# Kernel tuning notes

Hardware: AMD Instinct MI355X
Metric: run time of the kernel (lower is better)

## Reference

```python
import jax, jax.numpy as jnp
from jax import lax
import numpy as np

T, B, C, H, L, K = 512, 32, 512, 512, 2, 2  # time, batch, in_feat, hidden, layers, kernel


def setup_inputs() -> dict:
    key = jax.random.key(0)
    k0, k1, k2 = jax.random.split(key, 3)
    x = jax.random.normal(k0, (T, B, C), dtype=jnp.float32)
    # per layer: [n_dir=2, n_gate=4 (z,f,o,i), H, Cin, K] conv weights and [2,4,H] biases
    w0 = jax.random.normal(k1, (2, 4, H, C, K), dtype=jnp.float32) * 0.05
    b0 = jnp.zeros((2, 4, H), dtype=jnp.float32)
    w1 = jax.random.normal(k2, (2, 4, H, 2 * H, K), dtype=jnp.float32) * 0.05
    b1 = jnp.zeros((2, 4, H), dtype=jnp.float32)
    return {"x": x, "w0": w0, "b0": b0, "w1": w1, "b1": b1}


def _conv(x, w, b):
    # x: [B, Cin, T], w: [H, Cin, K]; left-pad K-1 zeros == torch cat([zeros, x]) + VALID conv
    y = lax.conv_general_dilated(x, w, (1,), [(K - 1, 0)],
                                 dimension_numbers=("NCH", "OIH", "NCH"))
    return y + b[None, :, None]


def _qrnn_layer(x, W, b, reverse):
    # x: [B, Cin, T]; W: [4, H, Cin, K]; b: [4, H]
    if reverse:
        x = x[:, :, ::-1]  # note: original code does NOT flip the output back
    z = jnp.tanh(_conv(x, W[0], b[0]))
    f = jax.nn.sigmoid(_conv(x, W[1], b[1]))  # eval-mode zoneout: 1-(1-sigmoid)=sigmoid
    o = jax.nn.sigmoid(_conv(x, W[2], b[2]))
    i = jax.nn.sigmoid(_conv(x, W[3], b[3]))
    iz = i * z
    f_t = jnp.moveaxis(f, 2, 0)   # [T, B, H]
    iz_t = jnp.moveaxis(iz, 2, 0)

    def step(c, fi):
        ft, izt = fi
        c = ft * c + izt  # IFO pooling recurrence
        return c, c

    _, cs = lax.scan(step, jnp.zeros(f_t.shape[1:], f.dtype), (f_t, iz_t))
    c = jnp.moveaxis(cs, 0, 2)  # [B, H, T]
    return o * c


def _forward(x, w0, b0, w1, b1):
    h = jnp.transpose(x, (1, 2, 0))  # [T,B,C] -> [B,C,T]
    h_lasts = []
    for W, bb in ((w0, b0), (w1, b1)):
        d0 = _qrnn_layer(h, W[0], bb[0], False)
        d1 = _qrnn_layer(h, W[1], bb[1], True)
        t_last = h.shape[2] - 2  # lengths.fill_(T-1); t_last = lengths - 1 = T-2 (faithful)
        h_lasts.append(jnp.concatenate([d0[:, :, t_last], d1[:, :, 0]], axis=1))  # [B, 2H]
        h = jnp.concatenate([d0, d1], axis=1)  # [B, 2H, T]
    output = jnp.transpose(h, (2, 0, 1))  # [T, B, 2H]
    h_n = jnp.stack(h_lasts, axis=0)      # [L, B, 2H]
    return output, h_n


def reference(x, w0, b0, w1, b1):
    return _forward(x, w0, b0, w1, b1)
```

## Files before the change

kernel.cpp:

```cpp
#include <hip/hip_runtime.h>
#include <cstddef>
#include <cstdint>

#define Tn 512
#define Bn 32
#define Hn 512
static const size_t PLANE = 8388608;

typedef float f32x4 __attribute__((ext_vector_type(4)));
typedef __bf16 bf16x8 __attribute__((ext_vector_type(8)));
typedef _Float16 h2 __attribute__((ext_vector_type(2)));

__device__ __forceinline__ float sigm(float x) { return 1.0f / (1.0f + __expf(-x)); }
__device__ __forceinline__ float tanh_fast(float x) { return 2.0f / (1.0f + __expf(-2.0f * x)) - 1.0f; }
__device__ __forceinline__ unsigned short f2bf(float f) {
    unsigned int u = __float_as_uint(f);
    u += 0x7FFF + ((u >> 16) & 1);
    return (unsigned short)(u >> 16);
}


__global__ __launch_bounds__(256) void conv_x(const float* __restrict__ x,
                                              unsigned short* __restrict__ xbf) {
    const int i = blockIdx.x * 256 + threadIdx.x;
    const int c8 = i & 63;
    const int tp = (i >> 6) % 514;
    const int b  = (i >> 6) / 514;
    unsigned short v[8];
    if (tp == 0 || tp == 513) {
#pragma unroll
        for (int j = 0; j < 8; ++j) v[j] = 0;
    } else {
        const float* s = x + ((size_t)(tp - 1) * Bn + b) * 512 + c8 * 8;
#pragma unroll
        for (int j = 0; j < 8; ++j) v[j] = f2bf(s[j]);
    }
    unsigned short* d = xbf + ((size_t)b * 514 + tp) * 512 + c8 * 8;
    *(uint4*)d = *(const uint4*)v;
}

__global__ __launch_bounds__(256) void conv_w2(const float* __restrict__ w0,
                                               const float* __restrict__ w1,
                                               unsigned short* __restrict__ w0bf,
                                               unsigned short* __restrict__ w1bf) {
    int i = blockIdx.x * 256 + threadIdx.x;
    const float* src;
    unsigned short* dst;
    int Cin;
    if (i < 4194304) { src = w0; dst = w0bf; Cin = 512; }
    else { i -= 4194304; src = w1; dst = w1bf; Cin = 1024; }
    const int K = 2 * Cin;
    const int dm2 = i / K;
    const int kp = i - dm2 * K;
    const int dir = dm2 >> 11;
    const int mp = dm2 & 2047;
    const int o = mp >> 2;
    const int g = mp & 3;
    const int tap = (kp >= Cin) ? 1 : 0;
    const int c = kp - tap * Cin;
    dst[i] = f2bf(src[((((size_t)dir * 4 + g) * 512 + o) * Cin + c) * 2 + tap]);
}

__global__ __launch_bounds__(256) void zero_h1pad(unsigned short* __restrict__ h1bf) {
    const int i = blockIdx.x * 256 + threadIdx.x;
    const int c = i & 1023;
    const int b = (i >> 10) & 31;
    const int tp = (i >> 15) ? 513 : 0;
    h1bf[((size_t)b * 514 + tp) * 1024 + c] = 0;
}

template <int CIN>
__global__ __launch_bounds__(512, 2) void gate_gemm_bf16(
    const unsigned short* __restrict__ Wbf,
    const unsigned short* __restrict__ Xbf,
    const float* __restrict__ bias,
    h2* __restrict__ fiz,
    _Float16* __restrict__ osb,
    float* __restrict__ Fsum,
    float* __restrict__ Ssum)
{
    __shared__ __align__(16) unsigned char smem[131072];
    unsigned short* lds0 = (unsigned short*)smem;

    const int tid = threadIdx.x;
    const int lane = tid & 63;
    const int wave = tid >> 6;
    const int wm = wave >> 2;
    const int wn = wave & 3;
    const int n0 = blockIdx.x * 256;
    const int dir = blockIdx.y >> 3;
    const int m0 = (blockIdx.y & 7) * 256;
    const int S32 = CIN / 32;
    const int NS = 2 * S32;
    const int dstep = dir ? -CIN : CIN;

    const unsigned short* Wb = Wbf + (size_t)dir * 2048 * 2 * CIN;

    const unsigned short* pA2[2];
    const unsigned short* pB2[2];
#pragma unroll
    for (int c = 0; c < 2; ++c) {
        const int row = c * 128 + (tid >> 2);
        const int kk = (tid & 3) ^ ((row >> 1) & 3);
        pA2[c] = Wb + (size_t)(m0 + row) * (2 * CIN) + kk * 8;
        const int n = n0 + row;
        const int t = n & 511;
        const int b = n >> 9;
        const int tp0 = dir ? (513 - t) : t;
        pB2[c] = Xbf + ((size_t)b * 514 + tp0) * CIN + kk * 8;
    }

    const int jr0 = lane >> 4;
    int offA[8], offB[4];
#pragma unroll
    for (int f = 0; f < 8; ++f) {
        const int ma = wm * 128 + f * 16 + (lane & 15);
        offA[f] = ma * 32 + (jr0 ^ ((ma >> 1) & 3)) * 8;
    }
#pragma unroll
    for (int f = 0; f < 4; ++f) {
        const int nb = wn * 64 + f * 16 + (lane & 15);
        offB[f] = nb * 32 + (jr0 ^ ((nb >> 1) & 3)) * 8;
    }

    f32x4 acc[8][4] = {};

#define GL(P, D) __builtin_amdgcn_global_load_lds( \
        (const __attribute__((address_space(1))) unsigned int*)(P), \
        (__attribute__((address_space(3))) unsigned int*)(D), 16, 0, 0)

#define STAGE(ks) do { \
    const int tap_ = ((ks) >= S32) ? 1 : 0; \
    const int aoff_ = tap_ * CIN + ((ks) - tap_ * S32) * 32; \
    const int boff_ = tap_ * dstep + ((ks) - tap_ * S32) * 32; \
    unsigned short* D_ = lds0 + ((ks) & 3) * 16384 + tid * 8; \
    GL(pA2[0] + aoff_, D_);          GL(pA2[1] + aoff_, D_ + 4096); \
    GL(pB2[0] + boff_, D_ + 8192);   GL(pB2[1] + boff_, D_ + 12288); \
} while (0)

#define RD_A(mh) do { \
    af[0] = *(const bf16x8*)&Ab[offA[(mh)*4+0]]; \
    af[1] = *(const bf16x8*)&Ab[offA[(mh)*4+1]]; \
    af[2] = *(const bf16x8*)&Ab[offA[(mh)*4+2]]; \
    af[3] = *(const bf16x8*)&Ab[offA[(mh)*4+3]]; \
} while (0)

#define RD_B() do { \
    bfr[0] = *(const bf16x8*)&Bb[offB[0]]; \
    bfr[1] = *(const bf16x8*)&Bb[offB[1]]; \
    bfr[2] = *(const bf16x8*)&Bb[offB[2]]; \
    bfr[3] = *(const bf16x8*)&Bb[offB[3]]; \
} while (0)

#define MM(mh) do { \
    _Pragma("unroll") \
    for (int f_ = 0; f_ < 4; ++f_) { \
        _Pragma("unroll") \
        for (int fn_ = 0; fn_ < 4; ++fn_) \
            acc[(mh)*4+f_][fn_] = __builtin_amdgcn_mfma_f32_16x16x32_bf16( \
                af[f_], bfr[fn_], acc[(mh)*4+f_][fn_], 0, 0, 0); \
    } \
} while (0)

    STAGE(0); STAGE(1); STAGE(2);
    asm volatile("s_waitcnt vmcnt(8)" ::: "memory");
    __builtin_amdgcn_s_barrier();

#pragma unroll 4
    for (int s = 0; s < NS; ++s) {
        asm volatile("" ::: "memory");
        const unsigned short* Ab = lds0 + (s & 3) * 16384;
        const unsigned short* Bb = Ab + 8192;
        bf16x8 af[4], bfr[4];
        RD_B(); RD_A(0);
        if (s + 3 < NS) STAGE(s + 3);
        __builtin_amdgcn_s_setprio(1);
        MM(0);
        RD_A(1);
        MM(1);
        __builtin_amdgcn_s_setprio(0);
        if (s + 3 < NS)      { asm volatile("s_waitcnt vmcnt(8)" ::: "memory"); }
        else if (s + 2 < NS) { asm volatile("s_waitcnt vmcnt(4)" ::: "memory"); }
        else if (s + 1 < NS) { asm volatile("s_waitcnt vmcnt(0)" ::: "memory"); }
        __builtin_amdgcn_s_barrier();
    }
#undef GL
#undef STAGE
#undef RD_A
#undef RD_B
#undef MM

    asm volatile("" ::: "memory");
    const int q4 = lane >> 4;
    const int o0 = (blockIdx.y & 7) * 64;
    const float* bb = bias + dir * 2048;
    h2* Lfiz = (h2*)smem;
    _Float16* Los = (_Float16*)(smem + 69632);
#pragma unroll
    for (int fm = 0; fm < 8; ++fm) {
        const int ol = wm * 32 + fm * 4 + q4;
        const int o = o0 + ol;
        const float Bz = bb[o];
        const float Bf = bb[512 + o];
        const float Bo = bb[1024 + o];
        const float Bi = bb[1536 + o];
#pragma unroll
        for (int fn = 0; fn < 4; ++fn) {
            f32x4 v = acc[fm][fn];
            const float fg = sigm(v.y + Bf);
            const float iz = sigm(v.w + Bi) * tanh_fast(v.x + Bz);
            const float og = sigm(v.z + Bo);
            const int nl = wn * 64 + fn * 16 + (lane & 15);
            h2 p; p.x = (_Float16)fg; p.y = (_Float16)iz;
            Lfiz[nl * 68 + ol] = p;
            Los[nl * 72 + ol] = (_Float16)og;
        }
    }
    __syncthreads();
    h2* fz = fiz + (size_t)dir * PLANE;
    _Float16* ob = osb + (size_t)dir * PLANE;
#pragma unroll
    for (int l = 0; l < 8; ++l) {
        const int idx = l * 512 + tid;
        const int row = idx >> 4;
        const int col = idx & 15;
        uint4 v = *(const uint4*)((const unsigned char*)smem + row * 272 + col * 16);
        ((uint4*)(fz + (size_t)(n0 + row) * 512 + o0))[col] = v;
    }
#pragma unroll
    for (int l = 0; l < 4; ++l) {
        const int idx = l * 512 + tid;
        const int row = idx >> 3;
        const int col = idx & 7;
        uint4 v = *(const uint4*)((const unsigned char*)smem + 69632 + row * 144 + col * 16);
        ((uint4*)(ob + (size_t)(n0 + row) * 512 + o0))[col] = v;
    }
    if (tid < 256) {
        const int ol = tid & 63;
        const int ch = tid >> 6;
        float F = 1.0f, S = 0.0f;
#pragma unroll
        for (int tt = 0; tt < 64; ++tt) {
            const h2 v = Lfiz[(ch * 64 + tt) * 68 + ol];
            const float fv = (float)v.x;
            F *= fv;
            S = fv * S + (float)v.y;
        }
        const int b = n0 >> 9;
        const int chg = ((n0 & 511) >> 6) + ch;
        const int o = o0 + ol;
        const int sidx = dir * 131072 + chg * 16384 + b * 512 + o;
        Fsum[sidx] = F;
        Ssum[sidx] = S;
    }
}


__global__ __launch_bounds__(256) void scan_B(
    const float* __restrict__ Fsum, const float* __restrict__ Ssum,
    float* __restrict__ cstart)
{
    const int i = blockIdx.x * 256 + threadIdx.x;
    const int base = (i >> 14) * 131072 + (i & 16383);
    float c = 0.0f;
    for (int ch = 0; ch < 8; ++ch) {
        cstart[base + ch * 16384] = c;
        c = Fsum[base + ch * 16384] * c + Ssum[base + ch * 16384];
    }
}

__global__ __launch_bounds__(256) void scan_C(
    const h2* __restrict__ fiz, const _Float16* __restrict__ osb,
    const float* __restrict__ cstart, float* __restrict__ out,
    unsigned short* __restrict__ h1bf,
    float* __restrict__ hn, int isLayer2)
{
    const int idx = blockIdx.x * 256 + threadIdx.x;
    const int dir = idx >> 17;
    const int rem = idx & 131071;
    const int o = rem & 511;
    const int b = (rem >> 9) & 31;
    const int chunk = rem >> 14;
    const int dirH = dir * 512;
    float c = cstart[idx];
    const h2* fz = fiz + (size_t)dir * PLANE;
    const _Float16* ob = osb + (size_t)dir * PLANE;
    const int tbase = chunk * 64;
    for (int tt = 0; tt < 64; ++tt) {
        const int t = tbase + tt;
        const size_t idxg = ((size_t)(b * 512 + t)) * 512 + o;
        const h2 v = fz[idxg];
        const float f = (float)v.x;
        const float iz = (float)v.y;
        const float os = (float)ob[idxg];
        c = f * c + iz;
        const float outv = os * c;
        if (isLayer2) {
            out[((size_t)t * Bn + b) * 1024 + dirH + o] = outv;
        } else {
            h1bf[((size_t)b * 514 + (t + 1)) * 1024 + dirH + o] = f2bf(outv);
        }
        const bool isLast = (dir == 0) ? (t == Tn - 2) : (t == 0);
        if (isLast) hn[(size_t)b * 1024 + dirH + o] = outv;
    }
}

extern "C" void kernel_launch(void* const* d_in, const int* in_sizes, int n_in,
                              void* d_out, int out_size, void* d_ws, size_t ws_size,
                              hipStream_t stream) {
    const float* x  = (const float*)d_in[0];
    const float* w0 = (const float*)d_in[1];
    const float* b0 = (const float*)d_in[2];
    const float* w1 = (const float*)d_in[3];
    const float* b1 = (const float*)d_in[4];
    float* out = (float*)d_out;
    float* ws = (float*)d_ws;

    h2* fiz        = (h2*)ws;
    _Float16* osb  = (_Float16*)(ws + 16777216);
    float* Fsum    = ws + 16777216 + 8388608;
    float* Ssum    = Fsum + 262144;
    float* cst     = Ssum + 262144;
    unsigned short* xbf  = (unsigned short*)(cst + 262144);
    unsigned short* h1bf = xbf + (size_t)32 * 514 * 512;
    unsigned short* w0bf = h1bf + (size_t)32 * 514 * 1024;
    unsigned short* w1bf = w0bf + (size_t)2 * 2048 * 1024;
    float* hn = out + 16777216;

    conv_x<<<4112, 256, 0, stream>>>(x, xbf);
    conv_w2<<<49152, 256, 0, stream>>>(w0, w1, w0bf, w1bf);
    zero_h1pad<<<256, 256, 0, stream>>>(h1bf);

    const dim3 gg(64, 16);

    gate_gemm_bf16<512><<<gg, 512, 0, stream>>>(w0bf, xbf, b0, fiz, osb, Fsum, Ssum);
    scan_B<<<128, 256, 0, stream>>>(Fsum, Ssum, cst);
    scan_C<<<1024, 256, 0, stream>>>(fiz, osb, cst, out, h1bf, hn, 0);
    gate_gemm_bf16<1024><<<gg, 512, 0, stream>>>(w1bf, h1bf, b1, fiz, osb, Fsum, Ssum);
    scan_B<<<128, 256, 0, stream>>>(Fsum, Ssum, cst);
    scan_C<<<1024, 256, 0, stream>>>(fiz, osb, cst, out, h1bf, hn + 32768, 1);
}
```

Measured before the change: 598.4 us.

## Load weight fragments directly from global into registers, bypassing LDS staging

The A operand (weights) is no longer staged through LDS. Each wave loads its MFMA A fragments straight from global memory into double-buffered registers one k-step ahead, and only the B (activation) tile goes through the LDS ring. This cuts LDS traffic and footprint and removes the A-side LDS reads. In exchange it raises register pressure (16 extra bf16x8 registers), loses the reuse of weights across waves that share the same rows, and makes global loads uncoalesced per lane. The vmcnt waits are retuned for the extra outstanding loads.

Result: slower. 1.126 ms (+88.1%).

```diff
diff --git a/kernel.cpp b/kernel.cpp
--- a/kernel.cpp
+++ b/kernel.cpp
@@ -79,7 +79,7 @@
     float* __restrict__ Fsum,
     float* __restrict__ Ssum)
 {
-    __shared__ __align__(16) unsigned char smem[131072];
+    __shared__ __align__(16) unsigned char smem[106496];
     unsigned short* lds0 = (unsigned short*)smem;
 
     const int tid = threadIdx.x;
@@ -96,13 +96,11 @@
 
     const unsigned short* Wb = Wbf + (size_t)dir * 2048 * 2 * CIN;
 
-    const unsigned short* pA2[2];
     const unsigned short* pB2[2];
 #pragma unroll
     for (int c = 0; c < 2; ++c) {
         const int row = c * 128 + (tid >> 2);
         const int kk = (tid & 3) ^ ((row >> 1) & 3);
-        pA2[c] = Wb + (size_t)(m0 + row) * (2 * CIN) + kk * 8;
         const int n = n0 + row;
         const int t = n & 511;
         const int b = n >> 9;
@@ -110,13 +108,14 @@
         pB2[c] = Xbf + ((size_t)b * 514 + tp0) * CIN + kk * 8;
     }
 
+    int offAg[8];
+#pragma unroll
+    for (int f = 0; f < 8; ++f) {
+        const int ma = m0 + wm * 128 + f * 16 + (lane & 15);
+        offAg[f] = ma * (2 * CIN) + (lane >> 4) * 8;
+    }
     const int jr0 = lane >> 4;
-    int offA[8], offB[4];
-#pragma unroll
-    for (int f = 0; f < 8; ++f) {
-        const int ma = wm * 128 + f * 16 + (lane & 15);
-        offA[f] = ma * 32 + (jr0 ^ ((ma >> 1) & 3)) * 8;
-    }
+    int offB[4];
 #pragma unroll
     for (int f = 0; f < 4; ++f) {
         const int nb = wn * 64 + f * 16 + (lane & 15);
@@ -124,6 +123,7 @@
     }
 
     f32x4 acc[8][4] = {};
+    bf16x8 aR0[8], aR1[8], bfr[4];
 
 #define GL(P, D) __builtin_amdgcn_global_load_lds( \
         (const __attribute__((address_space(1))) unsigned int*)(P), \
@@ -131,64 +131,58 @@
 
 #define STAGE(ks) do { \
     const int tap_ = ((ks) >= S32) ? 1 : 0; \
-    const int aoff_ = tap_ * CIN + ((ks) - tap_ * S32) * 32; \
     const int boff_ = tap_ * dstep + ((ks) - tap_ * S32) * 32; \
-    unsigned short* D_ = lds0 + ((ks) & 3) * 16384 + tid * 8; \
-    GL(pA2[0] + aoff_, D_);          GL(pA2[1] + aoff_, D_ + 4096); \
-    GL(pB2[0] + boff_, D_ + 8192);   GL(pB2[1] + boff_, D_ + 12288); \
+    unsigned short* D_ = lds0 + ((ks) & 3) * 8192 + tid * 8; \
+    GL(pB2[0] + boff_, D_);   GL(pB2[1] + boff_, D_ + 4096); \
 } while (0)
 
-#define RD_A(mh) do { \
-    af[0] = *(const bf16x8*)&Ab[offA[(mh)*4+0]]; \
-    af[1] = *(const bf16x8*)&Ab[offA[(mh)*4+1]]; \
-    af[2] = *(const bf16x8*)&Ab[offA[(mh)*4+2]]; \
-    af[3] = *(const bf16x8*)&Ab[offA[(mh)*4+3]]; \
-} while (0)
-
-#define RD_B() do { \
-    bfr[0] = *(const bf16x8*)&Bb[offB[0]]; \
-    bfr[1] = *(const bf16x8*)&Bb[offB[1]]; \
-    bfr[2] = *(const bf16x8*)&Bb[offB[2]]; \
-    bfr[3] = *(const bf16x8*)&Bb[offB[3]]; \
-} while (0)
-
-#define MM(mh) do { \
+#define BODY(ss, CUR, NXT) do { \
+    asm volatile("" ::: "memory"); \
+    if ((ss) + 1 < NS) { \
+        const unsigned short* Ap_ = Wb + (size_t)((ss) + 1) * 32; \
+        _Pragma("unroll") \
+        for (int f_ = 0; f_ < 8; ++f_) NXT[f_] = *(const bf16x8*)(Ap_ + offAg[f_]); \
+    } \
+    asm volatile("" ::: "memory"); \
+    if ((ss) + 3 < NS) STAGE((ss) + 3); \
+    asm volatile("" ::: "memory"); \
+    { const unsigned short* Bb_ = lds0 + ((ss) & 3) * 8192; \
+      bfr[0] = *(const bf16x8*)&Bb_[offB[0]]; \
+      bfr[1] = *(const bf16x8*)&Bb_[offB[1]]; \
+      bfr[2] = *(const bf16x8*)&Bb_[offB[2]]; \
+      bfr[3] = *(const bf16x8*)&Bb_[offB[3]]; } \
+    __builtin_amdgcn_s_setprio(1); \
     _Pragma("unroll") \
-    for (int f_ = 0; f_ < 4; ++f_) { \
+    for (int f_ = 0; f_ < 8; ++f_) { \
         _Pragma("unroll") \
         for (int fn_ = 0; fn_ < 4; ++fn_) \
-            acc[(mh)*4+f_][fn_] = __builtin_amdgcn_mfma_f32_16x16x32_bf16( \
-                af[f_], bfr[fn_], acc[(mh)*4+f_][fn_], 0, 0, 0); \
+            acc[f_][fn_] = __builtin_amdgcn_mfma_f32_16x16x32_bf16( \
+                CUR[f_], bfr[fn_], acc[f_][fn_], 0, 0, 0); \
     } \
+    __builtin_amdgcn_s_setprio(0); \
+    if ((ss) + 3 < NS)      { asm volatile("s_waitcnt vmcnt(12)" ::: "memory"); } \
+    else if ((ss) + 2 < NS) { asm volatile("s_waitcnt vmcnt(10)" ::: "memory"); } \
+    else if ((ss) + 1 < NS) { asm volatile("s_waitcnt vmcnt(8)" ::: "memory"); } \
+    if ((ss) + 1 < NS) __builtin_amdgcn_s_barrier(); \
 } while (0)
 
+    {
+        const unsigned short* Ap_ = Wb;
+#pragma unroll
+        for (int f_ = 0; f_ < 8; ++f_) aR0[f_] = *(const bf16x8*)(Ap_ + offAg[f_]);
+    }
+    asm volatile("" ::: "memory");
     STAGE(0); STAGE(1); STAGE(2);
-    asm volatile("s_waitcnt vmcnt(8)" ::: "memory");
+    asm volatile("s_waitcnt vmcnt(4)" ::: "memory");
     __builtin_amdgcn_s_barrier();
 
-#pragma unroll 4
-    for (int s = 0; s < NS; ++s) {
-        asm volatile("" ::: "memory");
-        const unsigned short* Ab = lds0 + (s & 3) * 16384;
-        const unsigned short* Bb = Ab + 8192;
-        bf16x8 af[4], bfr[4];
-        RD_B(); RD_A(0);
-        if (s + 3 < NS) STAGE(s + 3);
-        __builtin_amdgcn_s_setprio(1);
-        MM(0);
-        RD_A(1);
-        MM(1);
-        __builtin_amdgcn_s_setprio(0);
-        if (s + 3 < NS)      { asm volatile("s_waitcnt vmcnt(8)" ::: "memory"); }
-        else if (s + 2 < NS) { asm volatile("s_waitcnt vmcnt(4)" ::: "memory"); }
-        else if (s + 1 < NS) { asm volatile("s_waitcnt vmcnt(0)" ::: "memory"); }
-        __builtin_amdgcn_s_barrier();
+    for (int s = 0; s < NS; s += 2) {
+        BODY(s, aR0, aR1);
+        BODY(s + 1, aR1, aR0);
     }
 #undef GL
 #undef STAGE
-#undef RD_A
-#undef RD_B
-#undef MM
+#undef BODY
 
     asm volatile("" ::: "memory");
     const int q4 = lane >> 4;
```
